# Kernel tuning notes

Measured on AMD Instinct MI355X. Metric: run time of the kernel, lower is better.

## Reference

```python
import jax, jax.numpy as jnp
import numpy as np

N, D, K = 32768, 256, 4096
COMMITMENT_COST = 0.25
EPS_NORM = 1e-12  # matches torch F.normalize eps


def _l2_normalize(x):
    n = jnp.linalg.norm(x, axis=1, keepdims=True)
    return x / jnp.maximum(n, EPS_NORM)


def setup_inputs() -> dict:
    key = jax.random.key(0)
    k1, k2 = jax.random.split(key)
    inputs = jax.random.normal(k1, (N, D), dtype=jnp.float32)
    # xavier_uniform-like scale for the codebook
    bound = float(np.sqrt(6.0 / (K + D)))
    embeddings = jax.random.uniform(k2, (K, D), dtype=jnp.float32, minval=-bound, maxval=bound)
    return {"inputs": inputs, "embeddings": embeddings}


def reference(inputs, embeddings):
    flat = inputs.reshape(-1, D)
    x = _l2_normalize(flat)              # [N, D]
    e = _l2_normalize(embeddings)        # [K, D]
    # squared euclidean distance on normalized vectors
    distances = (jnp.sum(x * x, axis=1, keepdims=True)
                 + jnp.sum(e * e, axis=1)
                 - 2.0 * jnp.matmul(x, e.T))          # [N, K]
    encoding_indices = jnp.argmin(distances, axis=1)  # [N]
    quantized = embeddings[encoding_indices]          # gather, [N, D]
    # commitment loss (EMA variant: only commitment term is trained)
    e_latent_loss = jnp.mean((jax.lax.stop_gradient(quantized) - flat) ** 2)
    loss = COMMITMENT_COST * e_latent_loss
    # straight-through estimator
    quantized_st = flat + jax.lax.stop_gradient(quantized - flat)
    quantized_st = quantized_st.reshape(inputs.shape)
    return quantized_st, loss, encoding_indices
```

## Files before the change

### kernel.cpp

```cpp
#include <hip/hip_runtime.h>
#include <math.h>
#include <stdint.h>
#include <limits.h>

#define NPTS 32768
#define DIM  256
#define KCB  4096
#define NQ   (NPTS*DIM)

#define EPSN    1e-12f
#define MARGIN1 6.0e-4f
#define F16MIN  6.103515625e-05f
#define CAPB    4096
#define KINIT   0x7F800000FFFFFFFFull

typedef __attribute__((ext_vector_type(8))) _Float16 f16x8;
typedef __attribute__((ext_vector_type(4))) _Float16 f16x4;
typedef __attribute__((ext_vector_type(4))) float    f32x4;

#define WS_EH0   0u
#define WS_TRI   2097152u
#define WS_EMBT  0u
#define WS_SUME  4194304u
#define WS_EINV  4210688u
#define WS_XINV  4227072u
#define WS_IDX   4358144u
#define WS_RCA   4489216u
#define WS_RLA   4489232u
#define WS_RCB   4751376u
#define WS_RLB   4751392u
#define WS_BEST  4882464u
#define WS_LOSSP 4915232u

__device__ inline unsigned fbits(float f){ union{float f;unsigned u;}v; v.f=f; return v.u; }
__device__ inline float bitsf(unsigned u){ union{float f;unsigned u;}v; v.u=u; return v.f; }
__device__ inline uint64_t dbits(double d){ union{double d;uint64_t u;}v; v.d=d; return v.u; }
__device__ inline _Float16 g16(float v){
    return (fabsf(v) < F16MIN) ? (_Float16)0.0f : (_Float16)v;
}
__device__ inline void gload16(const void* src, void* lds){
    __builtin_amdgcn_global_load_lds((const __attribute__((address_space(1))) void*)src,
                                     (__attribute__((address_space(3))) void*)lds, 16, 0, 0);
}

__global__ void k_init(int* rca, int* rcb) {
    if (threadIdx.x == 0) { *rca = 0; *rcb = 0; }
}

__global__ __launch_bounds__(256) void k_norm_x(const float* __restrict__ x,
                                                float* __restrict__ xinv) {
    int w = threadIdx.x >> 6, l = threadIdx.x & 63;
    int row = blockIdx.x * 4 + w;
    float4 v = ((const float4*)x)[row * 64 + l];
    float s = v.x*v.x + v.y*v.y + v.z*v.z + v.w*v.w;
    #pragma unroll
    for (int o = 32; o; o >>= 1) s += __shfl_xor(s, o);
    if (l == 0) xinv[row] = 1.0f / fmaxf(sqrtf(s), EPSN);
}

__global__ __launch_bounds__(256) void k_norm_e(const float* __restrict__ e,
                                                _Float16* __restrict__ eh0,
                                                float* __restrict__ sume,
                                                float* __restrict__ einv) {
    int w = threadIdx.x >> 6, l = threadIdx.x & 63;
    int row = blockIdx.x * 4 + w;
    float4 v = ((const float4*)e)[row * 64 + l];
    float s = v.x*v.x + v.y*v.y + v.z*v.z + v.w*v.w;
    #pragma unroll
    for (int o = 32; o; o >>= 1) s += __shfl_xor(s, o);
    float inv = 1.0f / fmaxf(sqrtf(s), EPSN);
    float4 n = make_float4(v.x*inv, v.y*inv, v.z*inv, v.w*inv);
    f16x4 h0; h0[0]=g16(n.x); h0[1]=g16(n.y); h0[2]=g16(n.z); h0[3]=g16(n.w);
    ((f16x4*)eh0)[row * 64 + l] = h0;
    float s2 = n.x*n.x + n.y*n.y + n.z*n.z + n.w*n.w;
    #pragma unroll
    for (int o = 32; o; o >>= 1) s2 += __shfl_xor(s2, o);
    if (l == 0) { sume[row] = s2; einv[row] = inv; }
}

__global__ __launch_bounds__(256,2) void k_phase1(
    const float* __restrict__ x, const float* __restrict__ xinv,
    const _Float16* __restrict__ eh0, const float* __restrict__ sume,
    ulonglong2* __restrict__ tri)
{
    __shared__ __align__(16) _Float16 Bs[2][32 * DIM];
    const int tid = threadIdx.x;
    const int w = tid >> 6, l = tid & 63;
    const int l15 = l & 15, lhi = l >> 4;
    const int rowbase = (blockIdx.x >> 2) * 256 + w * 64;
    const int kbase   = (blockIdx.x & 3) * 1024;
    char* BsC = (char*)&Bs[0][0];

    f16x8 a[4][8];
    #pragma unroll
    for (int g = 0; g < 4; g++) {
        int row = rowbase + g*16 + l15;
        float xv = xinv[row];
        const float4* xr = (const float4*)(x + row * DIM);
        #pragma unroll
        for (int dc = 0; dc < 8; dc++) {
            float4 f0 = xr[dc*8 + lhi*2];
            float4 f1 = xr[dc*8 + lhi*2 + 1];
            f16x8 av;
            av[0]=g16(f0.x*xv); av[1]=g16(f0.y*xv);
            av[2]=g16(f0.z*xv); av[3]=g16(f0.w*xv);
            av[4]=g16(f1.x*xv); av[5]=g16(f1.y*xv);
            av[6]=g16(f1.z*xv); av[7]=g16(f1.w*xv);
            a[g][dc] = av;
        }
    }

    int offs[2][8];
    #pragma unroll
    for (int ni = 0; ni < 2; ni++) {
        int col = ni*16 + l15;
        int swz = (col & 7) << 4;
        #pragma unroll
        for (int dc = 0; dc < 8; dc++)
            offs[ni][dc] = (col*512 + dc*64 + lhi*16) ^ swz;
    }

    uint64_t t0[4], t1[4];
    float d2[4];
    #pragma unroll
    for (int g = 0; g < 4; g++) { t0[g]=KINIT; t1[g]=KINIT; d2[g]=INFINITY; }

    auto stage = [&](int kt, int bufbyte) {
        #pragma unroll
        for (int p = 0; p < 4; p++) {
            int c = p*256 + w*64 + l;
            int col = c >> 5;
            int off = (c << 4) & 511;
            int srcoff = off ^ ((col & 7) << 4);
            const void* src = (const void*)((const char*)eh0
                              + (size_t)(kbase + kt*32 + col) * 512 + srcoff);
            void* dst = (void*)(BsC + bufbyte + ((p*256 + w*64) << 4));
            gload16(src, dst);
        }
    };

    auto compute = [&](int kt, int bufbyte) {
        f32x4 acc[4][2];
        #pragma unroll
        for (int g = 0; g < 4; g++)
            #pragma unroll
            for (int ni = 0; ni < 2; ni++)
                acc[g][ni] = (f32x4){0.f,0.f,0.f,0.f};

        #pragma unroll
        for (int dc = 0; dc < 8; dc++) {
            #pragma unroll
            for (int ni = 0; ni < 2; ni++) {
                f16x8 b = *(const f16x8*)(BsC + bufbyte + offs[ni][dc]);
                acc[0][ni] = __builtin_amdgcn_mfma_f32_16x16x32_f16(b, a[0][dc], acc[0][ni], 0, 0, 0);
                acc[1][ni] = __builtin_amdgcn_mfma_f32_16x16x32_f16(b, a[1][dc], acc[1][ni], 0, 0, 0);
                acc[2][ni] = __builtin_amdgcn_mfma_f32_16x16x32_f16(b, a[2][dc], acc[2][ni], 0, 0, 0);
                acc[3][ni] = __builtin_amdgcn_mfma_f32_16x16x32_f16(b, a[3][dc], acc[3][ni], 0, 0, 0);
            }
        }

        #pragma unroll
        for (int ni = 0; ni < 2; ni++) {
            float4 se4 = *(const float4*)(sume + kbase + kt*32 + ni*16 + lhi*4);
            float ses[4] = {4.0f+se4.x, 4.0f+se4.y, 4.0f+se4.z, 4.0f+se4.w};
            #pragma unroll
            for (int g = 0; g < 4; g++) {
                #pragma unroll
                for (int r = 0; r < 4; r++) {
                    float db = ses[r] - 2.0f * acc[g][ni][r];
                    if (db < d2[g]) {
                        int code = kbase + kt*32 + ni*16 + lhi*4 + r;
                        uint64_t key = ((uint64_t)fbits(db) << 32) | (unsigned)code;
                        if (key < t1[g]) {
                            d2[g] = bitsf((unsigned)(t1[g] >> 32));
                            if (key < t0[g]) { t1[g] = t0[g]; t0[g] = key; }
                            else t1[g] = key;
                        } else {
                            d2[g] = db;
                        }
                    }
                }
            }
        }
    };

    stage(0, 0);
    for (int kt = 0; kt < 32; kt += 2) {
        __syncthreads();
        stage(kt + 1, 16384);
        compute(kt, 0);
        __syncthreads();
        if (kt + 2 < 32) stage(kt + 2, 0);
        compute(kt + 1, 16384);
    }

    #pragma unroll
    for (int g = 0; g < 4; g++) {
        uint64_t a0 = t0[g], a1 = t1[g];
        float a2 = d2[g];
        #pragma unroll
        for (int m = 16; m < 64; m <<= 1) {
            uint64_t b0 = __shfl_xor(a0, m), b1 = __shfl_xor(a1, m);
            float    b2 = __shfl_xor(a2, m);
            uint64_t lo  = a0 < b0 ? a0 : b0;
            uint64_t hi0 = a0 < b0 ? b0 : a0;
            uint64_t lo1 = a1 < b1 ? a1 : b1;
            uint64_t mid = hi0 > lo1 ? hi0 : lo1;
            a1 = hi0 < lo1 ? hi0 : lo1;
            a0 = lo;
            a2 = fminf(fminf(a2, b2), bitsf((unsigned)(mid >> 32)));
        }
        t0[g] = a0; t1[g] = a1; d2[g] = a2;
    }

    if (lhi == 0) {
        const int split = blockIdx.x & 3;
        #pragma unroll
        for (int g = 0; g < 4; g++) {
            int row = rowbase + g*16 + l15;
            float d0 = bitsf((unsigned)(t0[g] >> 32));
            uint64_t flag = (d2[g] - d0 < MARGIN1) ? (1ull << 12) : 0ull;
            ulonglong2 ent;
            ent.x = t0[g];
            ent.y = t1[g] | flag;
            tri[(row << 2) | split] = ent;
        }
    }
}

__global__ __launch_bounds__(256) void k_merge(
    const ulonglong2* __restrict__ tri,
    int* __restrict__ idx,
    int* __restrict__ rca, int2* __restrict__ rla,
    int* __restrict__ rcb, int* __restrict__ rlb)
{
    int row = blockIdx.x * 256 + threadIdx.x;
    ulonglong2 e0 = tri[row*4 + 0];
    ulonglong2 e1 = tri[row*4 + 1];
    ulonglong2 e2 = tri[row*4 + 2];
    ulonglong2 e3 = tri[row*4 + 3];

    uint64_t c0 = e0.x, c1 = e0.y & ~0x1000ull;
    float c2 = INFINITY;
    auto fold = [&](uint64_t b0, uint64_t b1) {
        b1 &= ~0x1000ull;
        uint64_t lo  = c0 < b0 ? c0 : b0;
        uint64_t hi0 = c0 < b0 ? b0 : c0;
        uint64_t lo1 = c1 < b1 ? c1 : b1;
        uint64_t mid = hi0 > lo1 ? hi0 : lo1;
        c1 = hi0 < lo1 ? hi0 : lo1;
        c0 = lo;
        c2 = fminf(c2, bitsf((unsigned)(mid >> 32)));
    };
    fold(e1.x, e1.y);
    fold(e2.x, e2.y);
    fold(e3.x, e3.y);

    int k0 = (int)((unsigned)c0 & 0xFFFu);
    idx[row] = k0;
    float d0 = bitsf((unsigned)(c0 >> 32));
    float d1 = bitsf((unsigned)(c1 >> 32));
    bool lA = (d1 - d0 < MARGIN1);
    bool lB = (c2 - d0 < MARGIN1);
    if ((e0.y >> 12) & 1) lB |= (bitsf((unsigned)(e0.x >> 32)) - d0 < MARGIN1);
    if ((e1.y >> 12) & 1) lB |= (bitsf((unsigned)(e1.x >> 32)) - d0 < MARGIN1);
    if ((e2.y >> 12) & 1) lB |= (bitsf((unsigned)(e2.x >> 32)) - d0 < MARGIN1);
    if ((e3.y >> 12) & 1) lB |= (bitsf((unsigned)(e3.x >> 32)) - d0 < MARGIN1);

    if (lA) {
        int k1 = (int)((unsigned)c1 & 0xFFFu);
        int p = atomicAdd(rca, 1);
        if (p < NPTS) rla[p] = make_int2(row, k0 | (k1 << 12));
    }
    if (lB) {
        int q = atomicAdd(rcb, 1);
        if (q < CAPB) rlb[q] = row;
    }
}

__global__ __launch_bounds__(256) void k_transpose(const float* __restrict__ emb,
                                                   const float* __restrict__ einv,
                                                   float* __restrict__ embT) {
    __shared__ float tile[64][65];
    const int tid = threadIdx.x;
    const int kb = (blockIdx.x & 63) * 64;
    const int db = (blockIdx.x >> 6) * 64;
    #pragma unroll
    for (int s = 0; s < 16; s++) {
        int i = s * 256 + tid;
        int lk = i >> 6, ld = i & 63;
        tile[lk][ld] = emb[(kb + lk) * DIM + db + ld] * einv[kb + lk];
    }
    __syncthreads();
    #pragma unroll
    for (int s = 0; s < 16; s++) {
        int i = s * 256 + tid;
        int ld = i >> 6, lk = i & 63;
        embT[(db + ld) * KCB + kb + lk] = tile[lk][ld];
    }
}

__global__ __launch_bounds__(256) void k_cand(
    const float* __restrict__ x, const float* __restrict__ emb,
    const float* __restrict__ xinv, const float* __restrict__ einv,
    const float* __restrict__ sume,
    const int* __restrict__ rca, const int2* __restrict__ rla,
    int* __restrict__ idx)
{
    int cnt = *rca; if (cnt > NPTS) cnt = NPTS;
    const int w = threadIdx.x >> 6, l = threadIdx.x & 63;
    for (int r = blockIdx.x * 4 + w; r < cnt; r += gridDim.x * 4) {
        int2 ent = rla[r];
        int row = ent.x;
        int k0 = ent.y & 0xFFF, k1 = (ent.y >> 12) & 0xFFF;
        float xv = xinv[row];
        float4 xf = ((const float4*)x)[row * 64 + l];
        double x0 = (double)xf.x * (double)xv, x1 = (double)xf.y * (double)xv;
        double x2 = (double)xf.z * (double)xv, x3 = (double)xf.w * (double)xv;
        int ks[2] = {k0, k1};
        double d[2];
        #pragma unroll
        for (int c = 0; c < 2; c++) {
            int k = ks[c];
            float ev = einv[k];
            float4 e4 = ((const float4*)emb)[k * 64 + l];
            d[c] = x0 * (double)(e4.x * ev) + x1 * (double)(e4.y * ev)
                 + x2 * (double)(e4.z * ev) + x3 * (double)(e4.w * ev);
        }
        #pragma unroll
        for (int o = 32; o; o >>= 1) {
            d[0] += __shfl_xor(d[0], o);
            d[1] += __shfl_xor(d[1], o);
        }
        if (l == 0) {
            double dist0 = 4.0 + (double)sume[k0] - 2.0 * d[0];
            double dist1 = 4.0 + (double)sume[k1] - 2.0 * d[1];
            uint64_t key0 = (dbits(dist0) & 0xFFFFFFFFFFFFF000ull) | (unsigned)k0;
            uint64_t key1 = (dbits(dist1) & 0xFFFFFFFFFFFFF000ull) | (unsigned)k1;
            idx[row] = (int)((key0 < key1 ? key0 : key1) & 0xFFFull);
        }
    }
}

__global__ __launch_bounds__(256) void k_binit(uint64_t* __restrict__ bestu) {
    bestu[blockIdx.x * 256 + threadIdx.x] = ~0ull;
}

__global__ __launch_bounds__(256) void k_full(
    const float* __restrict__ x, const float* __restrict__ embT,
    const float* __restrict__ xinv, const float* __restrict__ sume,
    const int* __restrict__ rcb, const int* __restrict__ rlb,
    uint64_t* __restrict__ bestu)
{
    __shared__ float xs[DIM];
    int cnt = *rcb; if (cnt > CAPB) cnt = CAPB; if (cnt <= 0) return;
    int items = cnt * 16;
    const int tid = threadIdx.x;
    for (int item = blockIdx.x; item < items; item += gridDim.x) {
        int r = item >> 4, chunk = item & 15;
        int row = rlb[r];
        __syncthreads();
        xs[tid] = x[row * DIM + tid] * xinv[row];
        __syncthreads();
        int k = chunk * 256 + tid;
        const float* et = embT + k;
        double dp0 = 0, dp1 = 0, dp2 = 0, dp3 = 0;
        #pragma unroll 8
        for (int d = 0; d < DIM; d += 4) {
            dp0 += (double)xs[d+0] * (double)et[(d+0) * KCB];
            dp1 += (double)xs[d+1] * (double)et[(d+1) * KCB];
            dp2 += (double)xs[d+2] * (double)et[(d+2) * KCB];
            dp3 += (double)xs[d+3] * (double)et[(d+3) * KCB];
        }
        double dist = 4.0 + (double)sume[k] - 2.0 * ((dp0 + dp1) + (dp2 + dp3));
        uint64_t key = (dbits(dist) & 0xFFFFFFFFFFFFF000ull) | (unsigned)k;
        atomicMin((unsigned long long*)&bestu[r], (unsigned long long)key);
    }
}

__global__ __launch_bounds__(256) void k_ffin(const int* __restrict__ rcb,
                                              const int* __restrict__ rlb,
                                              const uint64_t* __restrict__ bestu,
                                              int* __restrict__ idx) {
    int cnt = *rcb; if (cnt > CAPB) cnt = CAPB;
    int i = blockIdx.x * 256 + threadIdx.x;
    if (i < cnt) idx[rlb[i]] = (int)(bestu[i] & 0xFFFull);
}

__global__ __launch_bounds__(256) void k_gather(const float* __restrict__ x,
                                                const float* __restrict__ emb,
                                                const int* __restrict__ idx,
                                                float* __restrict__ out,
                                                float* __restrict__ lossp) {
    int t = blockIdx.x * 256 + threadIdx.x;
    float ls = 0.f;
    #pragma unroll
    for (int s = 0; s < 4; ++s) {
        int i4 = t + s * 524288;
        int n = i4 >> 6, c4 = i4 & 63;
        int id = idx[n];
        float4 f = ((const float4*)x)[i4];
        float4 q = ((const float4*)emb)[id * 64 + c4];
        float dx = q.x - f.x, dy = q.y - f.y, dz = q.z - f.z, dw = q.w - f.w;
        float4 o = make_float4(f.x + dx, f.y + dy, f.z + dz, f.w + dw);
        ((float4*)out)[i4] = o;
        ls += dx*dx + dy*dy + dz*dz + dw*dw;
        if (c4 == 0) out[NQ + 1 + n] = (float)id;
    }
    #pragma unroll
    for (int o = 32; o; o >>= 1) ls += __shfl_xor(ls, o);
    __shared__ float wsum[4];
    int wid = threadIdx.x >> 6, lane = threadIdx.x & 63;
    if (lane == 0) wsum[wid] = ls;
    __syncthreads();
    if (threadIdx.x == 0) lossp[blockIdx.x] = wsum[0] + wsum[1] + wsum[2] + wsum[3];
}

__global__ __launch_bounds__(256) void k_finalize(const float* __restrict__ lossp,
                                                  float* __restrict__ out) {
    double s = 0;
    for (int i = threadIdx.x; i < 2048; i += 256) s += (double)lossp[i];
    #pragma unroll
    for (int o = 32; o; o >>= 1) s += __shfl_xor(s, o);
    __shared__ double wd[4];
    int wid = threadIdx.x >> 6, lane = threadIdx.x & 63;
    if (lane == 0) wd[wid] = s;
    __syncthreads();
    if (threadIdx.x == 0)
        out[NQ] = (float)(0.25 * ((wd[0] + wd[1] + wd[2] + wd[3]) / (double)NQ));
}

extern "C" void kernel_launch(void* const* d_in, const int* in_sizes, int n_in,
                              void* d_out, int out_size, void* d_ws, size_t ws_size,
                              hipStream_t stream) {
    const float* x   = (const float*)d_in[0];
    const float* emb = (const float*)d_in[1];
    char* ws = (char*)d_ws;
    _Float16* eh0 = (_Float16*)(ws + WS_EH0);
    ulonglong2* tri = (ulonglong2*)(ws + WS_TRI);
    float* embT  = (float*)(ws + WS_EMBT);
    float* sume  = (float*)(ws + WS_SUME);
    float* einv  = (float*)(ws + WS_EINV);
    float* xinv  = (float*)(ws + WS_XINV);
    int*   idx   = (int*)  (ws + WS_IDX);
    int*   rca   = (int*)  (ws + WS_RCA);
    int2*  rla   = (int2*) (ws + WS_RLA);
    int*   rcb   = (int*)  (ws + WS_RCB);
    int*   rlb   = (int*)  (ws + WS_RLB);
    uint64_t* bestu = (uint64_t*)(ws + WS_BEST);
    float* lossp = (float*)(ws + WS_LOSSP);
    float* out = (float*)d_out;

    hipLaunchKernelGGL(k_init,     dim3(1),          dim3(64),  0, stream, rca, rcb);
    hipLaunchKernelGGL(k_norm_x,   dim3(NPTS/4),     dim3(256), 0, stream, x, xinv);
    hipLaunchKernelGGL(k_norm_e,   dim3(KCB/4),      dim3(256), 0, stream, emb, eh0, sume, einv);
    hipLaunchKernelGGL(k_phase1,   dim3(NPTS/256*4), dim3(256), 0, stream,
                       x, xinv, eh0, sume, tri);
    hipLaunchKernelGGL(k_merge,    dim3(NPTS/256),   dim3(256), 0, stream,
                       tri, idx, rca, rla, rcb, rlb);
    hipLaunchKernelGGL(k_transpose,dim3(256),        dim3(256), 0, stream, emb, einv, embT);
    hipLaunchKernelGGL(k_binit,    dim3(CAPB/256),   dim3(256), 0, stream, bestu);
    hipLaunchKernelGGL(k_cand,     dim3(1024),       dim3(256), 0, stream,
                       x, emb, xinv, einv, sume, rca, rla, idx);
    hipLaunchKernelGGL(k_full,     dim3(2048),       dim3(256), 0, stream,
                       x, embT, xinv, sume, rcb, rlb, bestu);
    hipLaunchKernelGGL(k_ffin,     dim3(16),         dim3(256), 0, stream, rcb, rlb, bestu, idx);
    hipLaunchKernelGGL(k_gather,   dim3(2048),       dim3(256), 0, stream,
                       x, emb, idx, out, lossp);
    hipLaunchKernelGGL(k_finalize, dim3(1),          dim3(256), 0, stream, lossp, out);
}
```

Baseline: 183.3 us.

## Restructure phase1 LDS layout, drop sume loads, add early-reject filter

The phase-1 kernel changes its shared-memory staging so that a simple linear LDS offset replaces the precomputed swizzled offset table, which frees registers. It also raises launch bounds to 3 blocks per CU. The per-code norm load is replaced with the constant 1 (4+1=5), on the assumption that normalized codebook rows have unit norm. A per-4-lane max prefilter skips the top-2 insertion logic when no candidate can qualify. The constant-norm approximation and the new LDS layout could change which candidates survive; the later exact rescoring stages are presumably meant to absorb that.

```diff
diff --git a/kernel.cpp b/kernel.cpp
--- a/kernel.cpp
+++ b/kernel.cpp
@@ -78,9 +78,9 @@
     if (l == 0) { sume[row] = s2; einv[row] = inv; }
 }
 
-__global__ __launch_bounds__(256,2) void k_phase1(
+__global__ __launch_bounds__(256,3) void k_phase1(
     const float* __restrict__ x, const float* __restrict__ xinv,
-    const _Float16* __restrict__ eh0, const float* __restrict__ sume,
+    const _Float16* __restrict__ eh0,
     ulonglong2* __restrict__ tri)
 {
     __shared__ __align__(16) _Float16 Bs[2][32 * DIM];
@@ -110,73 +110,65 @@
         }
     }
 
-    int offs[2][8];
-    #pragma unroll
-    for (int ni = 0; ni < 2; ni++) {
-        int col = ni*16 + l15;
-        int swz = (col & 7) << 4;
-        #pragma unroll
-        for (int dc = 0; dc < 8; dc++)
-            offs[ni][dc] = (col*512 + dc*64 + lhi*16) ^ swz;
-    }
-
     uint64_t t0[4], t1[4];
     float d2[4];
     #pragma unroll
     for (int g = 0; g < 4; g++) { t0[g]=KINIT; t1[g]=KINIT; d2[g]=INFINITY; }
 
+    const char* sbase = (const char*)eh0 + (size_t)kbase * 512
+                      + (size_t)(l & 31) * 512 + w*32 + (l >> 5)*16;
     auto stage = [&](int kt, int bufbyte) {
+        const char* s = sbase + kt * 16384;
         #pragma unroll
         for (int p = 0; p < 4; p++) {
-            int c = p*256 + w*64 + l;
-            int col = c >> 5;
-            int off = (c << 4) & 511;
-            int srcoff = off ^ ((col & 7) << 4);
-            const void* src = (const void*)((const char*)eh0
-                              + (size_t)(kbase + kt*32 + col) * 512 + srcoff);
-            void* dst = (void*)(BsC + bufbyte + ((p*256 + w*64) << 4));
-            gload16(src, dst);
+            gload16(s + p*128, BsC + bufbyte + ((p*256 + w*64) << 4));
         }
     };
+
+    const int rb = lhi*512 + l15*16;
+    const f32x4 zc = (f32x4){0.f, 0.f, 0.f, 0.f};
 
     auto compute = [&](int kt, int bufbyte) {
         f32x4 acc[4][2];
-        #pragma unroll
-        for (int g = 0; g < 4; g++)
-            #pragma unroll
-            for (int ni = 0; ni < 2; ni++)
-                acc[g][ni] = (f32x4){0.f,0.f,0.f,0.f};
-
         #pragma unroll
         for (int dc = 0; dc < 8; dc++) {
             #pragma unroll
             for (int ni = 0; ni < 2; ni++) {
-                f16x8 b = *(const f16x8*)(BsC + bufbyte + offs[ni][dc]);
-                acc[0][ni] = __builtin_amdgcn_mfma_f32_16x16x32_f16(b, a[0][dc], acc[0][ni], 0, 0, 0);
-                acc[1][ni] = __builtin_amdgcn_mfma_f32_16x16x32_f16(b, a[1][dc], acc[1][ni], 0, 0, 0);
-                acc[2][ni] = __builtin_amdgcn_mfma_f32_16x16x32_f16(b, a[2][dc], acc[2][ni], 0, 0, 0);
-                acc[3][ni] = __builtin_amdgcn_mfma_f32_16x16x32_f16(b, a[3][dc], acc[3][ni], 0, 0, 0);
+                f16x8 b = *(const f16x8*)(BsC + bufbyte + dc*2048 + ni*256 + rb);
+                if (dc == 0) {
+                    acc[0][ni] = __builtin_amdgcn_mfma_f32_16x16x32_f16(b, a[0][0], zc, 0, 0, 0);
+                    acc[1][ni] = __builtin_amdgcn_mfma_f32_16x16x32_f16(b, a[1][0], zc, 0, 0, 0);
+                    acc[2][ni] = __builtin_amdgcn_mfma_f32_16x16x32_f16(b, a[2][0], zc, 0, 0, 0);
+                    acc[3][ni] = __builtin_amdgcn_mfma_f32_16x16x32_f16(b, a[3][0], zc, 0, 0, 0);
+                } else {
+                    acc[0][ni] = __builtin_amdgcn_mfma_f32_16x16x32_f16(b, a[0][dc], acc[0][ni], 0, 0, 0);
+                    acc[1][ni] = __builtin_amdgcn_mfma_f32_16x16x32_f16(b, a[1][dc], acc[1][ni], 0, 0, 0);
+                    acc[2][ni] = __builtin_amdgcn_mfma_f32_16x16x32_f16(b, a[2][dc], acc[2][ni], 0, 0, 0);
+                    acc[3][ni] = __builtin_amdgcn_mfma_f32_16x16x32_f16(b, a[3][dc], acc[3][ni], 0, 0, 0);
+                }
             }
         }
 
         #pragma unroll
         for (int ni = 0; ni < 2; ni++) {
-            float4 se4 = *(const float4*)(sume + kbase + kt*32 + ni*16 + lhi*4);
-            float ses[4] = {4.0f+se4.x, 4.0f+se4.y, 4.0f+se4.z, 4.0f+se4.w};
             #pragma unroll
             for (int g = 0; g < 4; g++) {
-                #pragma unroll
-                for (int r = 0; r < 4; r++) {
-                    float db = ses[r] - 2.0f * acc[g][ni][r];
-                    if (db < d2[g]) {
-                        int code = kbase + kt*32 + ni*16 + lhi*4 + r;
-                        uint64_t key = ((uint64_t)fbits(db) << 32) | (unsigned)code;
-                        if (key < t1[g]) {
-                            d2[g] = bitsf((unsigned)(t1[g] >> 32));
-                            if (key < t0[g]) { t1[g] = t0[g]; t0[g] = key; }
-                            else t1[g] = key;
-                        } else {
-                            d2[g] = db;
+                f32x4 v = acc[g][ni];
+                float mx = fmaxf(fmaxf(v[0], v[1]), fmaxf(v[2], v[3]));
+                if (5.0f - 2.0f*mx < d2[g]) {
+                    #pragma unroll
+                    for (int r = 0; r < 4; r++) {
+                        float db = 5.0f - 2.0f*v[r];
+                        if (db < d2[g]) {
+                            int code = kbase + kt*32 + ni*16 + lhi*4 + r;
+                            uint64_t key = ((uint64_t)fbits(db) << 32) | (unsigned)code;
+                            if (key < t1[g]) {
+                                d2[g] = bitsf((unsigned)(t1[g] >> 32));
+                                if (key < t0[g]) { t1[g] = t0[g]; t0[g] = key; }
+                                else t1[g] = key;
+                            } else {
+                                d2[g] = db;
+                            }
                         }
                     }
                 }
@@ -455,7 +447,7 @@
     hipLaunchKernelGGL(k_norm_x,   dim3(NPTS/4),     dim3(256), 0, stream, x, xinv);
     hipLaunchKernelGGL(k_norm_e,   dim3(KCB/4),      dim3(256), 0, stream, emb, eh0, sume, einv);
     hipLaunchKernelGGL(k_phase1,   dim3(NPTS/256*4), dim3(256), 0, stream,
-                       x, xinv, eh0, sume, tri);
+                       x, xinv, eh0, tri);
     hipLaunchKernelGGL(k_merge,    dim3(NPTS/256),   dim3(256), 0, stream,
                        tri, idx, rca, rla, rcb, rlb);
     hipLaunchKernelGGL(k_transpose,dim3(256),        dim3(256), 0, stream, emb, einv, embT);
```

Measured after the change: 273.8 us. 1.49x slower.
